# Kernel tuning notes

Hardware: AMD Instinct MI355X
Metric: run time of the kernel (lower is better)

The kernel has to match this reference:

```python
import jax, jax.numpy as jnp
import numpy as np

EMBED_DIM = 512
NUM_HEADS = 8
HEAD_DIM = EMBED_DIM // NUM_HEADS


def setup_inputs() -> dict:
    key = jax.random.key(0)
    ks = jax.random.split(key, 9)
    d = EMBED_DIM
    s = 1.0 / np.sqrt(d)
    inp = {
        "x": jax.random.normal(ks[0], (2, 4096, d), dtype=jnp.float32),
        # torch nn.Linear weights are [out, in]; we store them the same way
        "Wq": jax.random.uniform(ks[1], (d, d), jnp.float32, -s, s),
        "bq": jax.random.uniform(ks[2], (d,), jnp.float32, -s, s),
        "Wk": jax.random.uniform(ks[3], (d, d), jnp.float32, -s, s),
        "bk": jax.random.uniform(ks[4], (d,), jnp.float32, -s, s),
        "Wv": jax.random.uniform(ks[5], (d, d), jnp.float32, -s, s),
        "bv": jax.random.uniform(ks[6], (d,), jnp.float32, -s, s),
        "Wo": jax.random.uniform(ks[7], (d, d), jnp.float32, -s, s),
        "bo": jax.random.uniform(ks[8], (d,), jnp.float32, -s, s),
    }
    return inp


def reference(x, Wq, bq, Wk, bk, Wv, bv, Wo, bo):
    B, S, D = x.shape
    H, Hd = NUM_HEADS, HEAD_DIM

    def proj(W, b):  # torch Linear: x @ W.T + b
        y = jnp.einsum("bsd,ed->bse", x, W) + b
        return y.reshape(B, S, H, Hd).transpose(0, 2, 1, 3)  # [B,H,S,Hd]

    Q = proj(Wq, bq)
    K = proj(Wk, bk)
    V = proj(Wv, bv)

    scale = 1.0 / jnp.sqrt(jnp.float32(Hd))
    scores = jnp.einsum("bhqd,bhkd->bhqk", Q, K) * scale  # [B,H,S,S]
    attn = jax.nn.softmax(scores, axis=-1)
    out = jnp.einsum("bhqk,bhkd->bhqd", attn, V)  # [B,H,S,Hd]
    out = out.transpose(0, 2, 1, 3).reshape(B, S, D)
    return jnp.einsum("bsd,ed->bse", out, Wo) + bo
```

## Files before the change

### kernel.cpp

```cpp
#include <hip/hip_runtime.h>


typedef unsigned short ushortT;
typedef __attribute__((ext_vector_type(8))) short short8;
typedef __attribute__((ext_vector_type(4))) float f32x4;
typedef __attribute__((ext_vector_type(16))) float f32x16;
typedef __attribute__((ext_vector_type(4))) unsigned int uint4v;
typedef __attribute__((ext_vector_type(2))) unsigned int uint2v;

__device__ __forceinline__ ushortT f2bf(float f) {
    unsigned int u = __builtin_bit_cast(unsigned int, f);
    u += 0x7FFFu + ((u >> 16) & 1u);
    return (ushortT)(u >> 16);
}

__device__ __forceinline__ unsigned int cvtpk(float lo, float hi) {
    unsigned int d;
    asm("v_cvt_pk_bf16_f32 %0, %1, %2" : "=v"(d) : "v"(lo), "v"(hi));
    return d;
}

__device__ __forceinline__ void plswap(unsigned int &a, unsigned int &b) {
    uint2v r = __builtin_amdgcn_permlane32_swap(a, b, false, false);
    a = r[0]; b = r[1];
}

#define GLDA 40
#define ALDK 72

__device__ __forceinline__ void stage_f32(ushortT* lds, const float* src)
{
    f32x4 a0 = *(const f32x4*)(src);
    f32x4 a1 = *(const f32x4*)(src + 4);
    short8 s;
    s[0] = (short)f2bf(a0[0]); s[1] = (short)f2bf(a0[1]);
    s[2] = (short)f2bf(a0[2]); s[3] = (short)f2bf(a0[3]);
    s[4] = (short)f2bf(a1[0]); s[5] = (short)f2bf(a1[1]);
    s[6] = (short)f2bf(a1[2]); s[7] = (short)f2bf(a1[3]);
    *(short8*)lds = s;
}

__global__ __launch_bounds__(256) void proj_qkv(
    const float* __restrict__ x,
    const float* __restrict__ Wq, const float* __restrict__ bq,
    const float* __restrict__ Wk, const float* __restrict__ bk,
    const float* __restrict__ Wv, const float* __restrict__ bv,
    ushortT* __restrict__ Qw, ushortT* __restrict__ Kw,
    ushortT* __restrict__ Vtw, float qscale)
{
    __shared__ __align__(16) ushortT As[128 * GLDA];
    __shared__ __align__(16) ushortT Bs[128 * GLDA];
    const int t = threadIdx.x;
    const int w = t >> 6, lane = t & 63;
    const int quad = lane >> 4, l15 = lane & 15;
    const int z = blockIdx.z;
    const int bx = blockIdx.x, by = blockIdx.y;
    const int wm = (w >> 1) * 64, wn = (w & 1) * 64;

    const float* W    = (z == 0) ? Wq : (z == 1) ? Wk : Wv;
    const float* bias = (z == 0) ? bq : (z == 1) ? bk : bv;
    const float* Asrc = (z < 2) ? x : W;
    const float* Bsrc = (z < 2) ? W : x;
    const int arow0 = (z < 2) ? bx * 128 : by * 128;
    const int brow0 = (z < 2) ? by * 128 : bx * 128;

    f32x4 acc[4][4] = {};

    for (int k0 = 0; k0 < 512; k0 += 32) {
#pragma unroll
        for (int i = 0; i < 2; i++) {
            int c = t + i * 256;
            int row = c >> 2, cc = c & 3;
            stage_f32(As + row * GLDA + cc * 8,
                      Asrc + (size_t)(arow0 + row) * 512 + k0 + cc * 8);
            stage_f32(Bs + row * GLDA + cc * 8,
                      Bsrc + (size_t)(brow0 + row) * 512 + k0 + cc * 8);
        }
        __syncthreads();
        short8 af[4], bfr[4];
#pragma unroll
        for (int i = 0; i < 4; i++)
            af[i] = *(const short8*)(As + (wm + i * 16 + l15) * GLDA + quad * 8);
#pragma unroll
        for (int i = 0; i < 4; i++)
            bfr[i] = *(const short8*)(Bs + (wn + i * 16 + l15) * GLDA + quad * 8);
#pragma unroll
        for (int mi = 0; mi < 4; mi++)
#pragma unroll
            for (int ni = 0; ni < 4; ni++)
                acc[mi][ni] = __builtin_amdgcn_mfma_f32_16x16x32_bf16(
                    af[mi], bfr[ni], acc[mi][ni], 0, 0, 0);
        __syncthreads();
    }

    if (z < 2) {
        ushortT* Y = (z == 0) ? Qw : Kw;
        const float sc = (z == 0) ? qscale : 1.0f;
#pragma unroll
        for (int ni = 0; ni < 4; ni++) {
            int col = brow0 + wn + ni * 16 + l15;
            float bv_ = bias[col];
#pragma unroll
            for (int mi = 0; mi < 4; mi++)
#pragma unroll
                for (int r = 0; r < 4; r++) {
                    int row = arow0 + wm + mi * 16 + quad * 4 + r;
                    Y[(size_t)row * 512 + col] = f2bf((acc[mi][ni][r] + bv_) * sc);
                }
        }
    } else {
        const int bidx = brow0 >> 12;
        const int s0 = brow0 & 4095;
#pragma unroll
        for (int mi = 0; mi < 4; mi++)
#pragma unroll
            for (int r = 0; r < 4; r++) {
                int ch = arow0 + wm + mi * 16 + quad * 4 + r;
                float bv_ = bias[ch];
#pragma unroll
                for (int ni = 0; ni < 4; ni++) {
                    int s = s0 + wn + ni * 16 + l15;
                    Vtw[(size_t)bidx * 2097152 + (size_t)ch * 4096 + s] =
                        f2bf(acc[mi][ni][r] + bv_);
                }
            }
    }
}

__global__ __launch_bounds__(256) void gemm_out(
    const ushortT* __restrict__ X, const float* __restrict__ W,
    const float* __restrict__ bias, float* __restrict__ Y)
{
    __shared__ __align__(16) ushortT As[128 * GLDA];
    __shared__ __align__(16) ushortT Bs[128 * GLDA];
    const int t = threadIdx.x;
    const int w = t >> 6, lane = t & 63;
    const int quad = lane >> 4, l15 = lane & 15;
    const int bm = blockIdx.x * 128, bn = blockIdx.y * 128;
    const int wm = (w >> 1) * 64, wn = (w & 1) * 64;

    f32x4 acc[4][4] = {};

    for (int k0 = 0; k0 < 512; k0 += 32) {
#pragma unroll
        for (int i = 0; i < 2; i++) {
            int c = t + i * 256;
            int row = c >> 2, cc = c & 3;
            *(uint4v*)(As + row * GLDA + cc * 8) =
                *(const uint4v*)(X + (size_t)(bm + row) * 512 + k0 + cc * 8);
            stage_f32(Bs + row * GLDA + cc * 8,
                      W + (size_t)(bn + row) * 512 + k0 + cc * 8);
        }
        __syncthreads();
        short8 af[4], bfr[4];
#pragma unroll
        for (int i = 0; i < 4; i++)
            af[i] = *(const short8*)(As + (wm + i * 16 + l15) * GLDA + quad * 8);
#pragma unroll
        for (int i = 0; i < 4; i++)
            bfr[i] = *(const short8*)(Bs + (wn + i * 16 + l15) * GLDA + quad * 8);
#pragma unroll
        for (int mi = 0; mi < 4; mi++)
#pragma unroll
            for (int ni = 0; ni < 4; ni++)
                acc[mi][ni] = __builtin_amdgcn_mfma_f32_16x16x32_bf16(
                    af[mi], bfr[ni], acc[mi][ni], 0, 0, 0);
        __syncthreads();
    }

#pragma unroll
    for (int ni = 0; ni < 4; ni++) {
        int col = bn + wn + ni * 16 + l15;
        float bv = bias[col];
#pragma unroll
        for (int mi = 0; mi < 4; mi++)
#pragma unroll
            for (int r = 0; r < 4; r++) {
                int row = bm + wm + mi * 16 + quad * 4 + r;
                Y[(size_t)row * 512 + col] = acc[mi][ni][r] + bv;
            }
    }
}

__global__ __launch_bounds__(256) void attn(
    const ushortT* Q, const ushortT* __restrict__ K,
    const ushortT* __restrict__ Vt, ushortT* O)
{
    __shared__ __align__(16) ushortT Ks[64 * ALDK];
    __shared__ __align__(16) ushortT Vs[64 * ALDK];

    const int t = threadIdx.x;
    const int w = t >> 6, lane = t & 63;
    const int l31 = lane & 31, hh = lane >> 5;
    const int qt = blockIdx.x, bh = blockIdx.y;
    const int b = bh >> 3, h = bh & 7;
    const size_t qrow = (size_t)b * 4096 + qt * 128 + w * 32 + l31;

    short8 qf[4];
    {
        const ushortT* qp = Q + qrow * 512 + h * 64 + hh * 8;
#pragma unroll
        for (int dk = 0; dk < 4; dk++)
            qf[dk] = *(const short8*)(qp + dk * 16);
    }

    f32x16 oacc[2] = {};
    float lpart = 0.f;

    const ushortT* Kbase = K + (size_t)b * 4096 * 512 + h * 64;
    const ushortT* Vbase = Vt + (size_t)b * 2097152 + (size_t)h * 64 * 4096;

    const int srow = t >> 3, scol = (t & 7) * 8;
    uint4v kg[2], vg[2];

#pragma unroll
    for (int i = 0; i < 2; i++) {
        kg[i] = *(const uint4v*)(Kbase + (size_t)(srow + 32 * i) * 512 + scol);
        vg[i] = *(const uint4v*)(Vbase + (size_t)(srow + 32 * i) * 4096 + scol);
    }
#pragma unroll
    for (int i = 0; i < 2; i++) {
        *(uint4v*)(Ks + (srow + 32 * i) * ALDK + scol) = kg[i];
        *(uint4v*)(Vs + (srow + 32 * i) * ALDK + scol) = vg[i];
    }

    for (int kt = 0; kt < 64; kt++) {
        __syncthreads();

        if (kt < 63) {
            const int kb = (kt + 1) * 64;
#pragma unroll
            for (int i = 0; i < 2; i++) {
                kg[i] = *(const uint4v*)(Kbase + (size_t)(kb + srow + 32 * i) * 512 + scol);
                vg[i] = *(const uint4v*)(Vbase + (size_t)(srow + 32 * i) * 4096 + kb + scol);
            }
        }

#pragma unroll
        for (int st = 0; st < 2; st++) {
            f32x16 sacc = {};
#pragma unroll
            for (int dk = 0; dk < 4; dk++) {
                short8 kf = *(const short8*)(Ks + (st * 32 + l31) * ALDK + dk * 16 + hh * 8);
                sacc = __builtin_amdgcn_mfma_f32_32x32x16_bf16(kf, qf[dk], sacc, 0, 0, 0);
            }
            float p[16];
#pragma unroll
            for (int r = 0; r < 16; r++) {
                p[r] = __builtin_amdgcn_exp2f(sacc[r]);
                lpart += p[r];
            }
            unsigned int c00 = cvtpk(p[0],  p[1]),  c01 = cvtpk(p[2],  p[3]);
            unsigned int c10 = cvtpk(p[4],  p[5]),  c11 = cvtpk(p[6],  p[7]);
            unsigned int c20 = cvtpk(p[8],  p[9]),  c21 = cvtpk(p[10], p[11]);
            unsigned int c30 = cvtpk(p[12], p[13]), c31 = cvtpk(p[14], p[15]);
            plswap(c00, c10);
            plswap(c01, c11);
            plswap(c20, c30);
            plswap(c21, c31);
            uint4v b0v = { c00, c01, c10, c11 };
            uint4v b1v = { c20, c21, c30, c31 };
            short8 B0 = __builtin_bit_cast(short8, b0v);
            short8 B1 = __builtin_bit_cast(short8, b1v);

#pragma unroll
            for (int dt = 0; dt < 2; dt++) {
                short8 vf0 = *(const short8*)(Vs + (dt * 32 + l31) * ALDK + st * 32 + hh * 8);
                short8 vf1 = *(const short8*)(Vs + (dt * 32 + l31) * ALDK + st * 32 + 16 + hh * 8);
                oacc[dt] = __builtin_amdgcn_mfma_f32_32x32x16_bf16(vf0, B0, oacc[dt], 0, 0, 0);
                oacc[dt] = __builtin_amdgcn_mfma_f32_32x32x16_bf16(vf1, B1, oacc[dt], 0, 0, 0);
            }
        }
        __syncthreads();

        if (kt < 63) {
#pragma unroll
            for (int i = 0; i < 2; i++) {
                *(uint4v*)(Ks + (srow + 32 * i) * ALDK + scol) = kg[i];
                *(uint4v*)(Vs + (srow + 32 * i) * ALDK + scol) = vg[i];
            }
        }
    }

    float l = lpart + __shfl_xor(lpart, 32);
    float rl = 1.0f / l;

    ushortT* orow = O + qrow * 512 + h * 64 + hh * 4;
#pragma unroll
    for (int dt = 0; dt < 2; dt++)
#pragma unroll
        for (int m = 0; m < 4; m++) {
            unsigned int u0 = cvtpk(oacc[dt][4 * m + 0] * rl, oacc[dt][4 * m + 1] * rl);
            unsigned int u1 = cvtpk(oacc[dt][4 * m + 2] * rl, oacc[dt][4 * m + 3] * rl);
            uint2v st2 = { u0, u1 };
            *(uint2v*)(orow + dt * 32 + m * 8) = st2;
        }
}

extern "C" void kernel_launch(void* const* d_in, const int* in_sizes, int n_in,
                              void* d_out, int out_size, void* d_ws, size_t ws_size,
                              hipStream_t stream)
{
    const float* x  = (const float*)d_in[0];
    const float* Wq = (const float*)d_in[1];
    const float* bq = (const float*)d_in[2];
    const float* Wk = (const float*)d_in[3];
    const float* bk = (const float*)d_in[4];
    const float* Wv = (const float*)d_in[5];
    const float* bv = (const float*)d_in[6];
    const float* Wo = (const float*)d_in[7];
    const float* bo = (const float*)d_in[8];

    ushortT* ws  = (ushortT*)d_ws;
    ushortT* Qw  = ws;
    ushortT* Kw  = ws + 4194304;
    ushortT* Vtw = ws + 2 * 4194304;

    const float qscale = 0.125f * 1.44269504089f;

    proj_qkv<<<dim3(64, 4, 3), 256, 0, stream>>>(
        x, Wq, bq, Wk, bk, Wv, bv, Qw, Kw, Vtw, qscale);
    attn<<<dim3(32, 16), 256, 0, stream>>>(Qw, Kw, Vtw, Qw);
    gemm_out<<<dim3(64, 4), 256, 0, stream>>>(Qw, Wo, bo, (float*)d_out);
}
```

Baseline: 223.2 us.

## Split attention KV sequence across two wave groups with double-buffered LDS

Each attention block now has 512 threads. The two halves of 256 threads each process half of the key/value sequence for the same 128 queries, and their partial outputs and row sums are combined through shared memory at the end. The K/V tiles are double-buffered in LDS, so there is one barrier per iteration instead of two. This doubles the number of waves working on the grid of 512 blocks, which raises occupancy on a GPU with many CUs, at the cost of four times the LDS per block and an extra reduction step.

```diff
diff --git a/kernel.cpp b/kernel.cpp
--- a/kernel.cpp
+++ b/kernel.cpp
@@ -182,19 +182,20 @@
     }
 }
 
-__global__ __launch_bounds__(256) void attn(
+__global__ __launch_bounds__(512) void attn(
     const ushortT* Q, const ushortT* __restrict__ K,
     const ushortT* __restrict__ Vt, ushortT* O)
 {
-    __shared__ __align__(16) ushortT Ks[64 * ALDK];
-    __shared__ __align__(16) ushortT Vs[64 * ALDK];
+    __shared__ __align__(16) ushortT Ks[2][2][64 * ALDK];
+    __shared__ __align__(16) ushortT Vs[2][2][64 * ALDK];
 
     const int t = threadIdx.x;
     const int w = t >> 6, lane = t & 63;
+    const int half = w >> 2, wq = w & 3;
     const int l31 = lane & 31, hh = lane >> 5;
     const int qt = blockIdx.x, bh = blockIdx.y;
     const int b = bh >> 3, h = bh & 7;
-    const size_t qrow = (size_t)b * 4096 + qt * 128 + w * 32 + l31;
+    const size_t qrow = (size_t)b * 4096 + qt * 128 + wq * 32 + l31;
 
     short8 qf[4];
     {
@@ -207,10 +208,12 @@
     f32x16 oacc[2] = {};
     float lpart = 0.f;
 
-    const ushortT* Kbase = K + (size_t)b * 4096 * 512 + h * 64;
-    const ushortT* Vbase = Vt + (size_t)b * 2097152 + (size_t)h * 64 * 4096;
-
-    const int srow = t >> 3, scol = (t & 7) * 8;
+    const int kofs = half * 2048;
+    const ushortT* Kbase = K + ((size_t)b * 4096 + kofs) * 512 + h * 64;
+    const ushortT* Vbase = Vt + (size_t)b * 2097152 + (size_t)h * 64 * 4096 + kofs;
+
+    const int th = t & 255;
+    const int srow = th >> 3, scol = (th & 7) * 8;
     uint4v kg[2], vg[2];
 
 #pragma unroll
@@ -220,14 +223,15 @@
     }
 #pragma unroll
     for (int i = 0; i < 2; i++) {
-        *(uint4v*)(Ks + (srow + 32 * i) * ALDK + scol) = kg[i];
-        *(uint4v*)(Vs + (srow + 32 * i) * ALDK + scol) = vg[i];
-    }
-
-    for (int kt = 0; kt < 64; kt++) {
-        __syncthreads();
-
-        if (kt < 63) {
+        *(uint4v*)(Ks[half][0] + (srow + 32 * i) * ALDK + scol) = kg[i];
+        *(uint4v*)(Vs[half][0] + (srow + 32 * i) * ALDK + scol) = vg[i];
+    }
+    __syncthreads();
+
+    for (int kt = 0; kt < 32; kt++) {
+        const int cur = kt & 1;
+
+        if (kt < 31) {
             const int kb = (kt + 1) * 64;
 #pragma unroll
             for (int i = 0; i < 2; i++) {
@@ -236,12 +240,15 @@
             }
         }
 
+        const ushortT* Kt = Ks[half][cur];
+        const ushortT* Vtl = Vs[half][cur];
+
 #pragma unroll
         for (int st = 0; st < 2; st++) {
             f32x16 sacc = {};
 #pragma unroll
             for (int dk = 0; dk < 4; dk++) {
-                short8 kf = *(const short8*)(Ks + (st * 32 + l31) * ALDK + dk * 16 + hh * 8);
+                short8 kf = *(const short8*)(Kt + (st * 32 + l31) * ALDK + dk * 16 + hh * 8);
                 sacc = __builtin_amdgcn_mfma_f32_32x32x16_bf16(kf, qf[dk], sacc, 0, 0, 0);
             }
             float p[16];
@@ -265,36 +272,59 @@
 
 #pragma unroll
             for (int dt = 0; dt < 2; dt++) {
-                short8 vf0 = *(const short8*)(Vs + (dt * 32 + l31) * ALDK + st * 32 + hh * 8);
-                short8 vf1 = *(const short8*)(Vs + (dt * 32 + l31) * ALDK + st * 32 + 16 + hh * 8);
+                short8 vf0 = *(const short8*)(Vtl + (dt * 32 + l31) * ALDK + st * 32 + hh * 8);
+                short8 vf1 = *(const short8*)(Vtl + (dt * 32 + l31) * ALDK + st * 32 + 16 + hh * 8);
                 oacc[dt] = __builtin_amdgcn_mfma_f32_32x32x16_bf16(vf0, B0, oacc[dt], 0, 0, 0);
                 oacc[dt] = __builtin_amdgcn_mfma_f32_32x32x16_bf16(vf1, B1, oacc[dt], 0, 0, 0);
             }
         }
-        __syncthreads();
-
-        if (kt < 63) {
+
+        if (kt < 31) {
+            const int nb = cur ^ 1;
 #pragma unroll
             for (int i = 0; i < 2; i++) {
-                *(uint4v*)(Ks + (srow + 32 * i) * ALDK + scol) = kg[i];
-                *(uint4v*)(Vs + (srow + 32 * i) * ALDK + scol) = vg[i];
-            }
-        }
-    }
-
-    float l = lpart + __shfl_xor(lpart, 32);
-    float rl = 1.0f / l;
-
-    ushortT* orow = O + qrow * 512 + h * 64 + hh * 4;
-#pragma unroll
-    for (int dt = 0; dt < 2; dt++)
-#pragma unroll
-        for (int m = 0; m < 4; m++) {
-            unsigned int u0 = cvtpk(oacc[dt][4 * m + 0] * rl, oacc[dt][4 * m + 1] * rl);
-            unsigned int u1 = cvtpk(oacc[dt][4 * m + 2] * rl, oacc[dt][4 * m + 3] * rl);
-            uint2v st2 = { u0, u1 };
-            *(uint2v*)(orow + dt * 32 + m * 8) = st2;
-        }
+                *(uint4v*)(Ks[half][nb] + (srow + 32 * i) * ALDK + scol) = kg[i];
+                *(uint4v*)(Vs[half][nb] + (srow + 32 * i) * ALDK + scol) = vg[i];
+            }
+        }
+        __syncthreads();
+    }
+
+    float* scratch = (float*)&Ks[0][0][0];
+    float* prow = scratch + (size_t)(wq * 64 + lane) * 36;
+
+    if (half == 1) {
+#pragma unroll
+        for (int dt = 0; dt < 2; dt++)
+#pragma unroll
+            for (int m = 0; m < 4; m++) {
+                f32x4 v4 = { oacc[dt][4 * m + 0], oacc[dt][4 * m + 1],
+                             oacc[dt][4 * m + 2], oacc[dt][4 * m + 3] };
+                *(f32x4*)(prow + dt * 16 + m * 4) = v4;
+            }
+        prow[32] = lpart;
+    }
+    __syncthreads();
+
+    if (half == 0) {
+        float sum = lpart + prow[32];
+        float l = sum + __shfl_xor(sum, 32);
+        float rl = 1.0f / l;
+
+        ushortT* orow = O + qrow * 512 + h * 64 + hh * 4;
+#pragma unroll
+        for (int dt = 0; dt < 2; dt++)
+#pragma unroll
+            for (int m = 0; m < 4; m++) {
+                f32x4 v4 = *(const f32x4*)(prow + dt * 16 + m * 4);
+                unsigned int u0 = cvtpk((oacc[dt][4 * m + 0] + v4[0]) * rl,
+                                        (oacc[dt][4 * m + 1] + v4[1]) * rl);
+                unsigned int u1 = cvtpk((oacc[dt][4 * m + 2] + v4[2]) * rl,
+                                        (oacc[dt][4 * m + 3] + v4[3]) * rl);
+                uint2v st2 = { u0, u1 };
+                *(uint2v*)(orow + dt * 32 + m * 8) = st2;
+            }
+    }
 }
 
 extern "C" void kernel_launch(void* const* d_in, const int* in_sizes, int n_in,
@@ -320,6 +350,6 @@
 
     proj_qkv<<<dim3(64, 4, 3), 256, 0, stream>>>(
         x, Wq, bq, Wk, bk, Wv, bv, Qw, Kw, Vtw, qscale);
-    attn<<<dim3(32, 16), 256, 0, stream>>>(Qw, Kw, Vtw, Qw);
+    attn<<<dim3(32, 16), 512, 0, stream>>>(Qw, Kw, Vtw, Qw);
     gemm_out<<<dim3(64, 4), 256, 0, stream>>>(Qw, Wo, bo, (float*)d_out);
 }
```

Result: faster. 218.6 us (-2.1%).
